# Kernel optimization log

Measured on AMD Instinct MI355X. Metric: run time of the kernel, lower is better.

Reference implementation:

```python
import jax, jax.numpy as jnp
import numpy as np

K_NEIGHBORS = 3


def setup_inputs() -> dict:
    key = jax.random.key(0)
    k1, k2 = jax.random.split(key)
    B, E, Hl, Wl = 8, 768, 32, 32   # ViT-Base latent grid for 512x512 / patch 16
    N = 20000                        # size of fitted kNN memory bank
    embeddings = jax.random.normal(k1, (B, E, Hl, Wl), dtype=jnp.float32)
    bank = jax.random.normal(k2, (N, E), dtype=jnp.float32)
    return {"embeddings": embeddings, "bank": bank, "out_size": 512}


def reference(embeddings, bank, out_size):
    # embeddings: [B, E, Hl, Wl]; bank: [N, E]
    B, E, Hl, Wl = embeddings.shape
    # permute(0,2,3,1) then flatten H,W -> queries [B, Hl*Wl, E]
    q = jnp.transpose(embeddings, (0, 2, 3, 1)).reshape(B, Hl * Wl, E)
    # squared Euclidean distances via ||q||^2 + ||b||^2 - 2 q.b
    q2 = jnp.sum(q * q, axis=-1, keepdims=True)            # [B, Q, 1]
    b2 = jnp.sum(bank * bank, axis=-1)                      # [N]
    d2 = q2 + b2[None, None, :] - 2.0 * jnp.einsum('bqe,ne->bqn', q, bank)  # [B, Q, N]
    # k nearest = top-k of negated squared distance
    neg_top, _ = jax.lax.top_k(-d2, K_NEIGHBORS)            # [B, Q, K]
    dist = jnp.sqrt(jnp.maximum(-neg_top, 1e-12))           # Euclidean distances
    scores = dist.mean(axis=-1).reshape(B, Hl, Wl)          # mean over k neighbors
    # F.interpolate(..., mode='bilinear') default align_corners=False == half-pixel
    out = jax.image.resize(scores[:, None, :, :], (B, 1, out_size, out_size), method='bilinear')
    return out
```

## Files before the change

### kernel.cpp

```cpp
#include <hip/hip_runtime.h>
#include <math.h>

#define KD     768
#define MT     64
#define NT     128
#define KB     128
#define NKC    6
#define NSPLIT 32
#define BIGF   3.0e38f

typedef __attribute__((ext_vector_type(4))) int   i32x4;
typedef __attribute__((ext_vector_type(8))) int   i32x8;
typedef __attribute__((ext_vector_type(4))) float f32x4;

__device__ __forceinline__ unsigned f2e4m3(float x) {
    unsigned u = __float_as_uint(x);
    unsigned s = (u >> 24) & 0x80u;
    float ax = __uint_as_float(u & 0x7fffffffu);
    if (ax < 0.015625f) {
        int n = (int)rintf(ax * 512.0f);
        if (n >= 8) return s | 0x08u;
        return s | (unsigned)n;
    }
    if (ax >= 464.0f) return s | 0x7Eu;
    unsigned m = __float_as_uint(ax);
    unsigned low = m & 0xFFFFFu;
    unsigned r = m >> 20;
    r += (low > 0x80000u) || (low == 0x80000u && (r & 1u));
    int ef = (int)(r >> 3) - 120;
    return s | ((unsigned)ef << 3) | (r & 7u);
}

__device__ __forceinline__ void ins3(float* t, float v) {
    float lo0 = fminf(t[0], v);
    float hi0 = fmaxf(t[0], v);
    float lo1 = fminf(t[1], hi0);
    float hi1 = fmaxf(t[1], hi0);
    float lo2 = fminf(t[2], hi1);
    t[0] = lo0; t[1] = lo1; t[2] = lo2;
}
__device__ __forceinline__ void async16(unsigned char* lds, const unsigned char* g) {
    __builtin_amdgcn_global_load_lds(
        (const __attribute__((address_space(1))) unsigned int*)g,
        (__attribute__((address_space(3))) unsigned int*)lds, 16, 0, 0);
}

__global__ void q_prep_k(const float* __restrict__ emb, unsigned char* __restrict__ qf8,
                         float* __restrict__ q2) {
    __shared__ float s[64][65];
    int bx  = blockIdx.x;
    int b   = bx / 192;
    int rem = bx % 192;
    int hw0 = (rem & 15) * 64;
    int eg  = rem >> 4;
    int e0  = eg * 64;
    const float* src = emb + (size_t)b * KD * 1024;
    unsigned int* q4 = (unsigned int*)qf8;
    #pragma unroll
    for (int i = 0; i < 16; ++i) {
        int idx = threadIdx.x + i * 256;
        int ee = idx >> 6, hh = idx & 63;
        s[ee][hh] = src[(size_t)(e0 + ee) * 1024 + hw0 + hh];
    }
    __syncthreads();
    #pragma unroll
    for (int i = 0; i < 4; ++i) {
        int slot = threadIdx.x + i * 256;
        int qq = slot >> 4, e4 = slot & 15;
        float v0 = s[e4 * 4 + 0][qq], v1 = s[e4 * 4 + 1][qq];
        float v2 = s[e4 * 4 + 2][qq], v3 = s[e4 * 4 + 3][qq];
        unsigned p = f2e4m3(v0) | (f2e4m3(v1) << 8)
                   | (f2e4m3(v2) << 16) | (f2e4m3(v3) << 24);
        q4[((size_t)b * 1024 + hw0 + qq) * (KD / 4) + e0 / 4 + e4] = p;
        float part = 0.f;
        part = fmaf(v0, v0, part); part = fmaf(v1, v1, part);
        part = fmaf(v2, v2, part); part = fmaf(v3, v3, part);
        #pragma unroll
        for (int off = 1; off < 16; off <<= 1) part += __shfl_xor(part, off, 64);
        if ((threadIdx.x & 15) == 0) atomicAdd(&q2[b * 1024 + hw0 + qq], part);
    }
}

__global__ void bank_prep_k(const float* __restrict__ bank, unsigned char* __restrict__ bf8,
                            float* __restrict__ b2, int N, int Npad) {
    int gid = blockIdx.x * 256 + threadIdx.x;
    int row = gid >> 6, lane = gid & 63;
    if (row >= Npad) return;
    unsigned int* b4 = (unsigned int*)bf8;
    if (row < N) {
        const float4* src = (const float4*)(bank + (size_t)row * KD);
        float s = 0.f;
        #pragma unroll
        for (int i = 0; i < KD / 256; ++i) {
            float4 v = src[lane + i * 64];
            s = fmaf(v.x, v.x, s); s = fmaf(v.y, v.y, s);
            s = fmaf(v.z, v.z, s); s = fmaf(v.w, v.w, s);
            unsigned p = f2e4m3(v.x) | (f2e4m3(v.y) << 8)
                       | (f2e4m3(v.z) << 16) | (f2e4m3(v.w) << 24);
            b4[(size_t)row * (KD / 4) + lane + i * 64] = p;
        }
        #pragma unroll
        for (int off = 32; off; off >>= 1) s += __shfl_down(s, off, 64);
        if (lane == 0) b2[row] = s;
    } else {
        #pragma unroll
        for (int i = 0; i < KD / 256; ++i) b4[(size_t)row * (KD / 4) + lane + i * 64] = 0;
        if (lane == 0) b2[row] = BIGF;
    }
}

__device__ __forceinline__ void stage_b(unsigned char* buf, const unsigned char* gB,
                                        int k0, int tid) {
    #pragma unroll
    for (int i = 0; i < 4; ++i) {
        int s = tid + i * 256;
        int m = s >> 3, g = s & 7;
        int G = g ^ (m & 7);
        async16(buf + s * 16, gB + (size_t)m * KD + k0 + G * 16);
    }
}

__device__ __forceinline__ i32x8 frag_read(const unsigned char* st, int base, int o0, int o1) {
    i32x4 lo = *(const i32x4*)&st[base + o0];
    i32x4 hi = *(const i32x4*)&st[base + o1];
    return __builtin_shufflevector(lo, hi, 0, 1, 2, 3, 4, 5, 6, 7);
}

__global__ __launch_bounds__(256, 2)
void knn_mfma_k(const unsigned char* __restrict__ qf8, const unsigned char* __restrict__ bf8,
                const float* __restrict__ b2g, float* __restrict__ cand,
                int ntiles, int Q) {
    __shared__ unsigned char bst[3][NT * KB];
    __shared__ float b2s[5 * NT];

    const int tid  = threadIdx.x;
    const int lane = tid & 63;
    const int quad = lane >> 4;
    const int l15  = lane & 15;
    const int wid  = tid >> 6;
    const int wm   = wid & 1;
    const int wn   = wid >> 1;
    const int xr   = l15 & 7;

    const int bx   = blockIdx.x;
    const int xcd  = bx & 7;
    const int rr_  = bx >> 9;
    const int jj   = (bx >> 3) & 63;
    const int mt   = xcd * 16 + (jj & 15);
    const int sp   = (jj >> 4) + 4 * rr_;
    const int Mbase = mt * MT;

    const int numnt = (ntiles - sp + NSPLIT - 1) / NSPLIT;

    for (int idx = tid; idx < numnt * NT; idx += 256) {
        int slot = idx >> 7, col = idx & 127;
        b2s[idx] = b2g[(size_t)(sp + slot * NSPLIT) * NT + col];
    }

    const unsigned char* gA = qf8 + ((size_t)Mbase + 32 * wm + l15) * KD + quad * 32;
    i32x8 af[NKC][2];
    #pragma unroll
    for (int kc = 0; kc < NKC; ++kc)
        #pragma unroll
        for (int mi = 0; mi < 2; ++mi) {
            const i32x4* p = (const i32x4*)(gA + (size_t)mi * 16 * KD + kc * KB);
            i32x4 lo = p[0];
            i32x4 hi = p[1];
            af[kc][mi] = __builtin_shufflevector(lo, hi, 0, 1, 2, 3, 4, 5, 6, 7);
        }

    float top3[24];
    #pragma unroll
    for (int i = 0; i < 24; ++i) top3[i] = BIGF;
    f32x4 acc[2][4];
    #pragma unroll
    for (int a = 0; a < 2; ++a)
        #pragma unroll
        for (int b = 0; b < 4; ++b) acc[a][b] = (f32x4){0.f, 0.f, 0.f, 0.f};

    const int o0 = ((2 * quad) ^ xr) * 16;
    const int o1 = ((2 * quad + 1) ^ xr) * 16;
    int bb[4];
    #pragma unroll
    for (int ni = 0; ni < 4; ++ni) bb[ni] = (64 * wn + 16 * ni + l15) * KB;

    __syncthreads();

    const unsigned char* gB0 = bf8 + (size_t)sp * NT * KD;
    stage_b(bst[0], gB0, 0, tid);
    stage_b(bst[1], gB0, KB, tid);

    for (int i = 0; i < numnt; ++i) {
        const unsigned char* gBc = bf8 + (size_t)(sp + i * NSPLIT) * NT * KD;
        const bool last = (i == numnt - 1);
        const unsigned char* gBn = last ? gBc
                                 : bf8 + (size_t)(sp + (i + 1) * NSPLIT) * NT * KD;
        #pragma unroll
        for (int kc = 0; kc < NKC; ++kc) {
            if (last && kc == NKC - 1) asm volatile("s_waitcnt vmcnt(0)" ::: "memory");
            else                       asm volatile("s_waitcnt vmcnt(4)" ::: "memory");
            __builtin_amdgcn_s_barrier();
            if (!(last && kc >= NKC - 2)) {
                if (kc < NKC - 2) stage_b(bst[(kc + 2) % 3], gBc, (kc + 2) * KB, tid);
                else              stage_b(bst[(kc + 2) % 3], gBn, (kc - 4) * KB, tid);
            }
            const unsigned char* st = bst[kc % 3];
            #pragma unroll
            for (int ni = 0; ni < 4; ++ni) {
                i32x8 bfr = frag_read(st, bb[ni], o0, o1);
                #pragma unroll
                for (int mi = 0; mi < 2; ++mi)
                    acc[mi][ni] = __builtin_amdgcn_mfma_scale_f32_16x16x128_f8f6f4(
                        af[kc][mi], bfr, acc[mi][ni], 0, 0,
                        0, 127, 0, 127);
            }
        }
        const float* b2p = &b2s[i * NT + 64 * wn];
        #pragma unroll
        for (int ni = 0; ni < 4; ++ni) {
            float b2v = b2p[16 * ni + l15];
            #pragma unroll
            for (int mi = 0; mi < 2; ++mi)
                #pragma unroll
                for (int r = 0; r < 4; ++r) {
                    float s = fmaf(-2.0f, acc[mi][ni][r], b2v);
                    ins3(&top3[(mi * 4 + r) * 3], s);
                }
        }
        #pragma unroll
        for (int a = 0; a < 2; ++a)
            #pragma unroll
            for (int b = 0; b < 4; ++b) acc[a][b] = (f32x4){0.f, 0.f, 0.f, 0.f};
    }

    #pragma unroll
    for (int mi = 0; mi < 2; ++mi)
        #pragma unroll
        for (int r = 0; r < 4; ++r) {
            float a0 = top3[(mi * 4 + r) * 3 + 0];
            float a1 = top3[(mi * 4 + r) * 3 + 1];
            float a2 = top3[(mi * 4 + r) * 3 + 2];
            #pragma unroll
            for (int off = 1; off < 16; off <<= 1) {
                float b0 = __shfl_xor(a0, off, 64);
                float b1 = __shfl_xor(a1, off, 64);
                float b2x = __shfl_xor(a2, off, 64);
                float t[3] = {a0, a1, a2};
                ins3(t, b0); ins3(t, b1); ins3(t, b2x);
                a0 = t[0]; a1 = t[1]; a2 = t[2];
            }
            if (l15 == 0) {
                int row = Mbase + 32 * wm + 16 * mi + 4 * quad + r;
                float* o = cand + ((size_t)(sp * 2 + wn) * Q + row) * 3;
                o[0] = a0; o[1] = a1; o[2] = a2;
            }
        }
}

__global__ void scores_k(const float* __restrict__ cand, const float* __restrict__ q2g,
                         float* __restrict__ scores, int Q) {
    int gid  = blockIdx.x * 256 + threadIdx.x;
    int q    = gid >> 6;
    int lane = gid & 63;
    if (q >= Q) return;
    const float* c = cand + ((size_t)lane * Q + q) * 3;
    float a0 = c[0], a1 = c[1], a2 = c[2];
    #pragma unroll
    for (int off = 1; off < 64; off <<= 1) {
        float b0 = __shfl_xor(a0, off, 64);
        float b1 = __shfl_xor(a1, off, 64);
        float b2x = __shfl_xor(a2, off, 64);
        float t[3] = {a0, a1, a2};
        ins3(t, b0); ins3(t, b1); ins3(t, b2x);
        a0 = t[0]; a1 = t[1]; a2 = t[2];
    }
    if (lane == 0) {
        float q2 = q2g[q];
        float s = (sqrtf(fmaxf(q2 + a0, 1e-12f)) +
                   sqrtf(fmaxf(q2 + a1, 1e-12f)) +
                   sqrtf(fmaxf(q2 + a2, 1e-12f))) * (1.f / 3.f);
        scores[q] = s;
    }
}

__global__ void upsample_k(const float* __restrict__ scores, float* __restrict__ out, int total) {
    int idx = blockIdx.x * blockDim.x + threadIdx.x;
    if (idx >= total) return;
    int x = idx & 511;
    int y = (idx >> 9) & 511;
    int b = idx >> 18;
    float sx = (x + 0.5f) * (1.f / 16.f) - 0.5f;
    float sy = (y + 0.5f) * (1.f / 16.f) - 0.5f;
    int x0 = (int)floorf(sx);
    int y0 = (int)floorf(sy);
    float wx = sx - (float)x0;
    float wy = sy - (float)y0;
    int x0c = min(max(x0, 0), 31), x1c = min(max(x0 + 1, 0), 31);
    int y0c = min(max(y0, 0), 31), y1c = min(max(y0 + 1, 0), 31);
    const float* sb = scores + (size_t)b * 1024;
    float v00 = sb[y0c * 32 + x0c], v01 = sb[y0c * 32 + x1c];
    float v10 = sb[y1c * 32 + x0c], v11 = sb[y1c * 32 + x1c];
    float v0 = v00 + wx * (v01 - v00);
    float v1 = v10 + wx * (v11 - v10);
    out[idx] = v0 + wy * (v1 - v0);
}

extern "C" void kernel_launch(void* const* d_in, const int* in_sizes, int n_in,
                              void* d_out, int out_size, void* d_ws, size_t ws_size,
                              hipStream_t stream) {
    const float* emb  = (const float*)d_in[0];
    const float* bank = (const float*)d_in[1];
    const int Q      = in_sizes[0] / KD;
    const int B      = Q / 1024;
    const int Nbank  = in_sizes[1] / KD;
    const int ntiles = (Nbank + NT - 1) / NT;
    const int Npad   = ntiles * NT;
    const int Mtiles = Q / MT;

    unsigned char* qf8 = (unsigned char*)d_ws;
    unsigned char* bf8 = qf8 + (size_t)Q * KD;
    float* fbase  = (float*)(bf8 + (size_t)Npad * KD);
    float* q2     = fbase;
    float* b2     = q2 + Q;
    float* cand   = b2 + Npad;
    float* scores = cand + (size_t)NSPLIT * 2 * Q * 3;
    float* out    = (float*)d_out;

    hipMemsetAsync(q2, 0, Q * sizeof(float), stream);
    hipLaunchKernelGGL(q_prep_k, dim3(B * 192), dim3(256), 0, stream, emb, qf8, q2);
    hipLaunchKernelGGL(bank_prep_k, dim3((Npad * 64 + 255) / 256), dim3(256), 0, stream,
                       bank, bf8, b2, Nbank, Npad);
    hipLaunchKernelGGL(knn_mfma_k, dim3(Mtiles * NSPLIT), dim3(256), 0, stream,
                       qf8, bf8, b2, cand, ntiles, Q);
    hipLaunchKernelGGL(scores_k, dim3((Q * 64 + 255) / 256), dim3(256), 0, stream,
                       cand, q2, scores, Q);
    hipLaunchKernelGGL(upsample_k, dim3((out_size + 255) / 256), dim3(256), 0, stream,
                       scores, out, out_size);
}
```

Before: 341.3 us.

## Switch bank staging to double-buffered 256-wide K windows with full waits

Replaces the three-slot ring of 128-wide K chunks with two ping-pong buffers that each hold a 256-wide K window. A block therefore syncs three times per bank tile instead of six. The fragment reads for the first half are issued before the next async stage, so the buffer can be overwritten safely. The trade-off is that each wait is now vmcnt(0), so the prefetch depth and the overlap between loads and MFMAs shrink. Register pressure also rises because eight B fragments are held at once.

```diff
diff --git a/kernel.cpp b/kernel.cpp
--- a/kernel.cpp
+++ b/kernel.cpp
@@ -109,15 +109,18 @@
     }
 }
 
-__device__ __forceinline__ void stage_b(unsigned char* buf, const unsigned char* gB,
+__device__ __forceinline__ void stage_w(unsigned char* buf, const unsigned char* gB,
                                         int k0, int tid) {
     #pragma unroll
-    for (int i = 0; i < 4; ++i) {
-        int s = tid + i * 256;
-        int m = s >> 3, g = s & 7;
-        int G = g ^ (m & 7);
-        async16(buf + s * 16, gB + (size_t)m * KD + k0 + G * 16);
-    }
+    for (int h = 0; h < 2; ++h)
+        #pragma unroll
+        for (int i = 0; i < 4; ++i) {
+            int s = tid + i * 256;
+            int m = s >> 3, g = s & 7;
+            int G = g ^ (m & 7);
+            async16(buf + h * (NT * KB) + s * 16,
+                    gB + (size_t)m * KD + k0 + h * KB + G * 16);
+        }
 }
 
 __device__ __forceinline__ i32x8 frag_read(const unsigned char* st, int base, int o0, int o1) {
@@ -130,7 +133,7 @@
 void knn_mfma_k(const unsigned char* __restrict__ qf8, const unsigned char* __restrict__ bf8,
                 const float* __restrict__ b2g, float* __restrict__ cand,
                 int ntiles, int Q) {
-    __shared__ unsigned char bst[3][NT * KB];
+    __shared__ unsigned char bst[2][2 * NT * KB];
     __shared__ float b2s[5 * NT];
 
     const int tid  = threadIdx.x;
@@ -187,33 +190,45 @@
     __syncthreads();
 
     const unsigned char* gB0 = bf8 + (size_t)sp * NT * KD;
-    stage_b(bst[0], gB0, 0, tid);
-    stage_b(bst[1], gB0, KB, tid);
-
+    stage_w(bst[0], gB0, 0, tid);
+
+    int pp = 0;
     for (int i = 0; i < numnt; ++i) {
         const unsigned char* gBc = bf8 + (size_t)(sp + i * NSPLIT) * NT * KD;
-        const bool last = (i == numnt - 1);
-        const unsigned char* gBn = last ? gBc
+        const bool lastt = (i == numnt - 1);
+        const unsigned char* gBn = lastt ? gBc
                                  : bf8 + (size_t)(sp + (i + 1) * NSPLIT) * NT * KD;
         #pragma unroll
-        for (int kc = 0; kc < NKC; ++kc) {
-            if (last && kc == NKC - 1) asm volatile("s_waitcnt vmcnt(0)" ::: "memory");
-            else                       asm volatile("s_waitcnt vmcnt(4)" ::: "memory");
+        for (int w = 0; w < 3; ++w) {
+            asm volatile("s_waitcnt vmcnt(0)" ::: "memory");
             __builtin_amdgcn_s_barrier();
-            if (!(last && kc >= NKC - 2)) {
-                if (kc < NKC - 2) stage_b(bst[(kc + 2) % 3], gBc, (kc + 2) * KB, tid);
-                else              stage_b(bst[(kc + 2) % 3], gBn, (kc - 4) * KB, tid);
+            const unsigned char* st = bst[pp];
+            i32x8 ba[4];
+            #pragma unroll
+            for (int ni = 0; ni < 4; ++ni) ba[ni] = frag_read(st, bb[ni], o0, o1);
+            if (!(lastt && w == 2)) {
+                if (w < 2) stage_w(bst[pp ^ 1], gBc, (2 * w + 2) * KB, tid);
+                else       stage_w(bst[pp ^ 1], gBn, 0, tid);
             }
-            const unsigned char* st = bst[kc % 3];
-            #pragma unroll
-            for (int ni = 0; ni < 4; ++ni) {
-                i32x8 bfr = frag_read(st, bb[ni], o0, o1);
+            i32x8 bbf[4];
+            #pragma unroll
+            for (int ni = 0; ni < 4; ++ni)
+                bbf[ni] = frag_read(st + NT * KB, bb[ni], o0, o1);
+            #pragma unroll
+            for (int ni = 0; ni < 4; ++ni)
                 #pragma unroll
                 for (int mi = 0; mi < 2; ++mi)
                     acc[mi][ni] = __builtin_amdgcn_mfma_scale_f32_16x16x128_f8f6f4(
-                        af[kc][mi], bfr, acc[mi][ni], 0, 0,
+                        af[2 * w][mi], ba[ni], acc[mi][ni], 0, 0,
                         0, 127, 0, 127);
-            }
+            #pragma unroll
+            for (int ni = 0; ni < 4; ++ni)
+                #pragma unroll
+                for (int mi = 0; mi < 2; ++mi)
+                    acc[mi][ni] = __builtin_amdgcn_mfma_scale_f32_16x16x128_f8f6f4(
+                        af[2 * w + 1][mi], bbf[ni], acc[mi][ni], 0, 0,
+                        0, 127, 0, 127);
+            pp ^= 1;
         }
         const float* b2p = &b2s[i * NT + 64 * wn];
         #pragma unroll
```

After: 315.4 us. -7.6%, faster.

## Give each wave its own bank slice with private double-buffered LDS staging

Applied to the files above, without the earlier changes.

The block tile changes from 64 queries x 128 bank rows to 32 queries x 256 bank rows. Each of the four waves now loads and consumes its own 64-row slice of bank fp8 data through a private double buffer, which removes the block-wide s_barrier per K-chunk. The split count halves so the grid shape and the 64 candidate partitions per query stay the same. In exchange, each bank element staged in LDS is reused by fewer query rows, so global and LDS traffic per MFMA goes up, and there is less prefetch depth (2 buffers instead of 3).

```diff
diff --git a/kernel.cpp b/kernel.cpp
--- a/kernel.cpp
+++ b/kernel.cpp
@@ -2,11 +2,11 @@
 #include <math.h>
 
 #define KD     768
-#define MT     64
-#define NT     128
+#define MT     32
+#define NT     256
 #define KB     128
 #define NKC    6
-#define NSPLIT 32
+#define NSPLIT 16
 #define BIGF   3.0e38f
 
 typedef __attribute__((ext_vector_type(4))) int   i32x4;
@@ -109,11 +109,11 @@
     }
 }
 
-__device__ __forceinline__ void stage_b(unsigned char* buf, const unsigned char* gB,
-                                        int k0, int tid) {
-    #pragma unroll
-    for (int i = 0; i < 4; ++i) {
-        int s = tid + i * 256;
+__device__ __forceinline__ void stage_slice(unsigned char* buf, const unsigned char* gB,
+                                            int k0, int lane) {
+    #pragma unroll
+    for (int i = 0; i < 8; ++i) {
+        int s = lane + i * 64;
         int m = s >> 3, g = s & 7;
         int G = g ^ (m & 7);
         async16(buf + s * 16, gB + (size_t)m * KD + k0 + G * 16);
@@ -130,34 +130,32 @@
 void knn_mfma_k(const unsigned char* __restrict__ qf8, const unsigned char* __restrict__ bf8,
                 const float* __restrict__ b2g, float* __restrict__ cand,
                 int ntiles, int Q) {
-    __shared__ unsigned char bst[3][NT * KB];
+    __shared__ unsigned char bst[4][2][64 * KB];
     __shared__ float b2s[5 * NT];
 
     const int tid  = threadIdx.x;
     const int lane = tid & 63;
     const int quad = lane >> 4;
     const int l15  = lane & 15;
-    const int wid  = tid >> 6;
-    const int wm   = wid & 1;
-    const int wn   = wid >> 1;
+    const int wv   = tid >> 6;
     const int xr   = l15 & 7;
 
     const int bx   = blockIdx.x;
     const int xcd  = bx & 7;
     const int rr_  = bx >> 9;
     const int jj   = (bx >> 3) & 63;
-    const int mt   = xcd * 16 + (jj & 15);
-    const int sp   = (jj >> 4) + 4 * rr_;
+    const int mt   = xcd * 32 + (jj & 31);
+    const int sp   = (jj >> 5) + 2 * rr_;
     const int Mbase = mt * MT;
 
     const int numnt = (ntiles - sp + NSPLIT - 1) / NSPLIT;
 
     for (int idx = tid; idx < numnt * NT; idx += 256) {
-        int slot = idx >> 7, col = idx & 127;
+        int slot = idx >> 8, col = idx & 255;
         b2s[idx] = b2g[(size_t)(sp + slot * NSPLIT) * NT + col];
     }
 
-    const unsigned char* gA = qf8 + ((size_t)Mbase + 32 * wm + l15) * KD + quad * 32;
+    const unsigned char* gA = qf8 + ((size_t)Mbase + l15) * KD + quad * 32;
     i32x8 af[NKC][2];
     #pragma unroll
     for (int kc = 0; kc < NKC; ++kc)
@@ -180,42 +178,46 @@
 
     const int o0 = ((2 * quad) ^ xr) * 16;
     const int o1 = ((2 * quad + 1) ^ xr) * 16;
-    int bb[4];
-    #pragma unroll
-    for (int ni = 0; ni < 4; ++ni) bb[ni] = (64 * wn + 16 * ni + l15) * KB;
+
+    unsigned char* my0 = &bst[wv][0][0];
+    unsigned char* my1 = &bst[wv][1][0];
 
     __syncthreads();
 
-    const unsigned char* gB0 = bf8 + (size_t)sp * NT * KD;
-    stage_b(bst[0], gB0, 0, tid);
-    stage_b(bst[1], gB0, KB, tid);
-
+    const unsigned char* gB0 = bf8 + ((size_t)sp * NT + wv * 64) * KD;
+    stage_slice(my0, gB0, 0, lane);
+
+    int pp = 0;
     for (int i = 0; i < numnt; ++i) {
-        const unsigned char* gBc = bf8 + (size_t)(sp + i * NSPLIT) * NT * KD;
-        const bool last = (i == numnt - 1);
-        const unsigned char* gBn = last ? gBc
-                                 : bf8 + (size_t)(sp + (i + 1) * NSPLIT) * NT * KD;
+        const unsigned char* gBc = bf8 + ((size_t)(sp + i * NSPLIT) * NT + wv * 64) * KD;
+        const bool lastt = (i == numnt - 1);
+        const unsigned char* gBn = lastt ? gBc
+            : bf8 + ((size_t)(sp + (i + 1) * NSPLIT) * NT + wv * 64) * KD;
         #pragma unroll
         for (int kc = 0; kc < NKC; ++kc) {
-            if (last && kc == NKC - 1) asm volatile("s_waitcnt vmcnt(0)" ::: "memory");
-            else                       asm volatile("s_waitcnt vmcnt(4)" ::: "memory");
-            __builtin_amdgcn_s_barrier();
-            if (!(last && kc >= NKC - 2)) {
-                if (kc < NKC - 2) stage_b(bst[(kc + 2) % 3], gBc, (kc + 2) * KB, tid);
-                else              stage_b(bst[(kc + 2) % 3], gBn, (kc - 4) * KB, tid);
+            if (!(lastt && kc == NKC - 1)) {
+                unsigned char* nbuf = pp ? my0 : my1;
+                if (kc < NKC - 1) stage_slice(nbuf, gBc, (kc + 1) * KB, lane);
+                else              stage_slice(nbuf, gBn, 0, lane);
+                asm volatile("s_waitcnt vmcnt(8)" ::: "memory");
+            } else {
+                asm volatile("s_waitcnt vmcnt(0)" ::: "memory");
             }
-            const unsigned char* st = bst[kc % 3];
-            #pragma unroll
-            for (int ni = 0; ni < 4; ++ni) {
-                i32x8 bfr = frag_read(st, bb[ni], o0, o1);
+            const unsigned char* st = pp ? my1 : my0;
+            i32x8 bfr[4];
+            #pragma unroll
+            for (int ni = 0; ni < 4; ++ni)
+                bfr[ni] = frag_read(st, (16 * ni + l15) * KB, o0, o1);
+            #pragma unroll
+            for (int ni = 0; ni < 4; ++ni)
                 #pragma unroll
                 for (int mi = 0; mi < 2; ++mi)
                     acc[mi][ni] = __builtin_amdgcn_mfma_scale_f32_16x16x128_f8f6f4(
-                        af[kc][mi], bfr, acc[mi][ni], 0, 0,
+                        af[kc][mi], bfr[ni], acc[mi][ni], 0, 0,
                         0, 127, 0, 127);
-            }
-        }
-        const float* b2p = &b2s[i * NT + 64 * wn];
+            pp ^= 1;
+        }
+        const float* b2p = &b2s[i * NT + wv * 64];
         #pragma unroll
         for (int ni = 0; ni < 4; ++ni) {
             float b2v = b2p[16 * ni + l15];
@@ -250,8 +252,8 @@
                 a0 = t[0]; a1 = t[1]; a2 = t[2];
             }
             if (l15 == 0) {
-                int row = Mbase + 32 * wm + 16 * mi + 4 * quad + r;
-                float* o = cand + ((size_t)(sp * 2 + wn) * Q + row) * 3;
+                int row = Mbase + 16 * mi + 4 * quad + r;
+                float* o = cand + ((size_t)(sp * 4 + wv) * Q + row) * 3;
                 o[0] = a0; o[1] = a1; o[2] = a2;
             }
         }
@@ -323,7 +325,7 @@
     float* q2     = fbase;
     float* b2     = q2 + Q;
     float* cand   = b2 + Npad;
-    float* scores = cand + (size_t)NSPLIT * 2 * Q * 3;
+    float* scores = cand + (size_t)64 * Q * 3;
     float* out    = (float*)d_out;
 
     hipMemsetAsync(q2, 0, Q * sizeof(float), stream);
```

After: 350.9 us. +2.8%, slower.
